# Optimization experiments

Hardware: AMD Instinct MI355X
Metric: run time of the kernel (lower is better)

## Reference

```python
import jax, jax.numpy as jnp
import numpy as np

EPS = 1e-6

def fexp(x, p):
    # signed power used in superquadric parametrization
    return jnp.sign(x) * (jnp.abs(x) + EPS) ** p

def quat_to_rot(q):
    q = q / (jnp.linalg.norm(q, axis=-1, keepdims=True) + EPS)
    w, x, y, z = q[..., 0], q[..., 1], q[..., 2], q[..., 3]
    R = jnp.stack([
        jnp.stack([1 - 2 * (y * y + z * z), 2 * (x * y - w * z), 2 * (x * z + w * y)], -1),
        jnp.stack([2 * (x * y + w * z), 1 - 2 * (x * x + z * z), 2 * (y * z - w * x)], -1),
        jnp.stack([2 * (x * z - w * y), 2 * (y * z + w * x), 1 - 2 * (x * x + y * y)], -1),
    ], -2)
    return R  # (..., 3, 3)

def setup_inputs() -> dict:
    key = jax.random.key(0)
    ks = jax.random.split(key, 9)
    B, M, S, N = 8, 16, 100, 2048
    pcl = jax.random.normal(ks[0], (B, N, 3), jnp.float32)
    translations = 0.5 * jax.random.normal(ks[1], (B, M, 3), jnp.float32)
    rotations = jax.random.normal(ks[2], (B, M, 4), jnp.float32)
    size = 0.2 + 0.6 * jax.random.uniform(ks[3], (B, M, 3), jnp.float32)
    shape_eps = 0.4 + 1.2 * jax.random.uniform(ks[4], (B, M, 2), jnp.float32)
    deformations = 0.6 * jax.random.uniform(ks[5], (B, M, 2), jnp.float32) - 0.3
    probabilities = jax.random.uniform(ks[6], (B, M), jnp.float32, 0.05, 0.95)
    etas = jax.random.uniform(ks[7], (S,), jnp.float32, -np.pi / 2, np.pi / 2)
    omegas = jax.random.uniform(ks[8], (S,), jnp.float32, -np.pi, np.pi)
    return {"pcl": pcl, "translations": translations, "rotations": rotations,
            "size": size, "shape_eps": shape_eps, "deformations": deformations,
            "probabilities": probabilities, "etas": etas, "omegas": omegas}

def reference(pcl, translations, rotations, size, shape_eps, deformations, probabilities, etas, omegas):
    B, N, _ = pcl.shape
    M = translations.shape[1]
    # transform pcl into primitive-centric frames: (B,N,M,3)
    R = quat_to_rot(rotations)                                   # (B,M,3,3)
    d = pcl[:, :, None, :] - translations[:, None, :, :]         # (B,N,M,3)
    pcl_t = jnp.einsum('bmij,bnmj->bnmi', R, d)                  # (B,N,M,3)
    # sample superquadric surfaces: (B,M,S,3)
    e1 = shape_eps[..., 0:1]; e2 = shape_eps[..., 1:2]           # (B,M,1)
    a1 = size[..., 0:1]; a2 = size[..., 1:2]; a3 = size[..., 2:3]
    ce = fexp(jnp.cos(etas)[None, None, :], e1)
    se = fexp(jnp.sin(etas)[None, None, :], e1)
    cw = fexp(jnp.cos(omegas)[None, None, :], e2)
    sw = fexp(jnp.sin(omegas)[None, None, :], e2)
    x = a1 * ce * cw; y = a2 * ce * sw; z = a3 * se              # (B,M,S)
    # tapering deformation
    fx = deformations[..., 0:1] * z / a3 + 1.0
    fy = deformations[..., 1:2] * z / a3 + 1.0
    points = jnp.stack([fx * x, fy * y, z], -1)                  # (B,M,S,3)
    # pairwise squared distances: (B,M,S,N)
    diff = points[:, :, :, None, :] - jnp.transpose(pcl_t, (0, 2, 1, 3))[:, :, None, :, :]
    dist = jnp.sum(diff * diff, -1)
    # --- pcl_to_prim loss ---
    dmin = jnp.transpose(jnp.min(dist, axis=2), (0, 2, 1))       # (B,N,M)
    idx = jnp.argsort(dmin, axis=-1)
    distance = jnp.take_along_axis(dmin, idx, axis=-1)
    probs_g = jax.vmap(lambda p, i: p[i])(probabilities, idx)    # (B,N,M)
    neg_cp = jnp.cumprod(1.0 - probs_g, axis=-1)
    neg_cp = jnp.concatenate([jnp.ones_like(neg_cp[..., :1]), neg_cp[..., :-1]], -1)
    minprob = probs_g * neg_cp
    pcl_to_prim = jnp.sum(distance * minprob) / (B * N)
    # --- prim_to_pcl loss ---
    dminN = jnp.min(dist, axis=3)                                # (B,M,S)
    dminN = jnp.where(dminN >= 1e30, 0.0, dminN)
    s0, s1, s2 = size[..., 0], size[..., 1], size[..., 2]
    area = 4 * np.pi * ((s0 * s1) ** 1.6 / 3 + (s0 * s2) ** 1.6 / 3 + (s1 * s2) ** 1.6 / 3) ** 0.625
    area = M * area / jnp.sum(area, axis=-1, keepdims=True)
    prim_to_pcl = jnp.sum(jnp.mean(dminN, -1) * area) / (B * M)
    # regularizer weights are zero (regularizer_type=None path) -> regs = 0
    return pcl_to_prim + prim_to_pcl
```

## Files before the change

### kernel.cpp

```cpp
#include <hip/hip_runtime.h>
#include <math.h>

#define EPSF 1e-6f

constexpr int B = 8, N = 2048, M = 16, S = 100;
constexpr int MAIN_BLOCKS = B * (N / 64);
constexpr int PRIM_BLOCKS = B * M * 2;
constexpr int TOTAL_BLOCKS = MAIN_BLOCKS + PRIM_BLOCKS;
constexpr int NPART = MAIN_BLOCKS * 4 + PRIM_BLOCKS;

typedef float v2f __attribute__((ext_vector_type(2)));

__device__ __forceinline__ float hw_exp2(float x) { return __builtin_amdgcn_exp2f(x); }
__device__ __forceinline__ float hw_log2(float x) { return __builtin_amdgcn_logf(x); }

__device__ __forceinline__ float fexp_d(float x, float p) {
    float sg = (x > 0.f) ? 1.f : ((x < 0.f) ? -1.f : 0.f);
    return sg * __powf(fabsf(x) + EPSF, p);
}

__device__ __forceinline__ float sgn_d(float x) {
    return (x > 0.f) ? 1.f : ((x < 0.f) ? -1.f : 0.f);
}

__device__ __forceinline__ void quat_R(const float* __restrict__ rot, int bm, float R[9]) {
    float w = rot[bm * 4 + 0], x = rot[bm * 4 + 1], y = rot[bm * 4 + 2], z = rot[bm * 4 + 3];
    float inv = 1.0f / (sqrtf(w * w + x * x + y * y + z * z) + EPSF);
    w *= inv; x *= inv; y *= inv; z *= inv;
    R[0] = 1.f - 2.f * (y * y + z * z); R[1] = 2.f * (x * y - w * z); R[2] = 2.f * (x * z + w * y);
    R[3] = 2.f * (x * y + w * z); R[4] = 1.f - 2.f * (x * x + z * z); R[5] = 2.f * (y * z - w * x);
    R[6] = 2.f * (x * z - w * y); R[7] = 2.f * (y * z + w * x); R[8] = 1.f - 2.f * (x * x + y * y);
}

__device__ __forceinline__ float4 surf_point(
    const float* __restrict__ sizep, const float* __restrict__ seps,
    const float* __restrict__ deform, const float* __restrict__ etas,
    const float* __restrict__ omegas, int bm, int s)
{
    float e1 = seps[bm * 2 + 0], e2 = seps[bm * 2 + 1];
    float a1 = sizep[bm * 3 + 0], a2 = sizep[bm * 3 + 1], a3 = sizep[bm * 3 + 2];
    float d0 = deform[bm * 2 + 0], d1 = deform[bm * 2 + 1];
    float se_, ce_, sw_, cw_;
    __sincosf(etas[s], &se_, &ce_);
    __sincosf(omegas[s], &sw_, &cw_);
    float ce = fexp_d(ce_, e1);
    float se = fexp_d(se_, e1);
    float cw = fexp_d(cw_, e2);
    float sw = fexp_d(sw_, e2);
    float x = a1 * ce * cw;
    float y = a2 * ce * sw;
    float z = a3 * se;
    float fx = d0 * (z / a3) + 1.0f;
    float fy = d1 * (z / a3) + 1.0f;
    float4 P;
    P.x = fx * x; P.y = fy * y; P.z = z;
    P.w = P.x * P.x + P.y * P.y + P.z * P.z;
    return P;
}

__global__ __launch_bounds__(256) void k_all(
    const float* __restrict__ pcl, const float* __restrict__ trans,
    const float* __restrict__ rot, const float* __restrict__ sizep,
    const float* __restrict__ seps, const float* __restrict__ deform,
    const float* __restrict__ probs,
    const float* __restrict__ etas, const float* __restrict__ omegas,
    float* __restrict__ part, unsigned int* __restrict__ flags,
    float* __restrict__ out)
{
    __shared__ float4 pts[S * M];
    __shared__ float trig[S * 8];
    __shared__ float sbuf[20];

    int t = threadIdx.x;

    if (blockIdx.x < MAIN_BLOCKS) {
        int b  = blockIdx.x >> 5;
        int n0 = (blockIdx.x & 31) * 64;

        if (t < S) {
            float se_, ce_, sw_, cw_;
            __sincosf(etas[t], &se_, &ce_);
            __sincosf(omegas[t], &sw_, &cw_);
            trig[t * 8 + 0] = hw_log2(fabsf(ce_) + EPSF);
            trig[t * 8 + 1] = sgn_d(ce_);
            trig[t * 8 + 2] = hw_log2(fabsf(se_) + EPSF);
            trig[t * 8 + 3] = sgn_d(se_);
            trig[t * 8 + 4] = hw_log2(fabsf(cw_) + EPSF);
            trig[t * 8 + 5] = sgn_d(cw_);
            trig[t * 8 + 6] = hw_log2(fabsf(sw_) + EPSF);
            trig[t * 8 + 7] = sgn_d(sw_);
        }
        __syncthreads();

        for (int i = t; i < S * M; i += 256) {
            int s = i >> 4, mm = i & 15;
            int bmi = b * M + mm;
            float e1 = seps[bmi * 2 + 0], e2 = seps[bmi * 2 + 1];
            float a1 = sizep[bmi * 3 + 0], a2 = sizep[bmi * 3 + 1], a3 = sizep[bmi * 3 + 2];
            float d0 = deform[bmi * 2 + 0], d1 = deform[bmi * 2 + 1];
            float ce = trig[s * 8 + 1] * hw_exp2(e1 * trig[s * 8 + 0]);
            float se = trig[s * 8 + 3] * hw_exp2(e1 * trig[s * 8 + 2]);
            float cw = trig[s * 8 + 5] * hw_exp2(e2 * trig[s * 8 + 4]);
            float sw = trig[s * 8 + 7] * hw_exp2(e2 * trig[s * 8 + 6]);
            float x = a1 * ce * cw;
            float y = a2 * ce * sw;
            float z = a3 * se;
            float fx = fmaf(d0, se, 1.0f);
            float fy = fmaf(d1, se, 1.0f);
            float4 P;
            P.x = fx * x; P.y = fy * y; P.z = z;
            P.w = P.x * P.x + P.y * P.y + P.z * P.z;
            pts[i] = P;
        }
        __syncthreads();

        int m  = t & 15;
        int nl = t >> 4;
        int bm = b * M + m;
        float R[9];
        quat_R(rot, bm, R);
        float tx = trans[bm * 3 + 0], ty = trans[bm * 3 + 1], tz = trans[bm * 3 + 2];

        v2f mx2[2], my2[2], mz2[2], dmin2[2];
        float psq[4];
#pragma unroll
        for (int j = 0; j < 4; j++) {
            int n = n0 + nl + 16 * j;
            float px = pcl[(b * N + n) * 3 + 0];
            float py = pcl[(b * N + n) * 3 + 1];
            float pz = pcl[(b * N + n) * 3 + 2];
            float dx = px - tx, dy = py - ty, dz = pz - tz;
            float X = R[0] * dx + R[1] * dy + R[2] * dz;
            float Y = R[3] * dx + R[4] * dy + R[5] * dz;
            float Z = R[6] * dx + R[7] * dy + R[8] * dz;
            mx2[j >> 1][j & 1] = -2.f * X;
            my2[j >> 1][j & 1] = -2.f * Y;
            mz2[j >> 1][j & 1] = -2.f * Z;
            psq[j] = X * X + Y * Y + Z * Z;
            dmin2[j >> 1][j & 1] = 3.4e38f;
        }

        auto compute4 = [&](const float4* P4) {
#pragma unroll
            for (int u = 0; u < 4; u++) {
                float4 P = P4[u];
                v2f vx = {P.x, P.x}, vy = {P.y, P.y}, vz = {P.z, P.z}, vw = {P.w, P.w};
#pragma unroll
                for (int p = 0; p < 2; p++) {
                    v2f d = __builtin_elementwise_fma(vx, mx2[p], vw);
                    d = __builtin_elementwise_fma(vy, my2[p], d);
                    d = __builtin_elementwise_fma(vz, mz2[p], d);
                    dmin2[p] = __builtin_elementwise_min(dmin2[p], d);
                }
            }
        };

        float4 Pa[4], Pb[4];
#pragma unroll
        for (int u = 0; u < 4; u++) Pa[u] = pts[u * M + m];
        for (int g = 0; g < 24; g += 2) {
#pragma unroll
            for (int u = 0; u < 4; u++) Pb[u] = pts[(4 * (g + 1) + u) * M + m];
            compute4(Pa);
#pragma unroll
            for (int u = 0; u < 4; u++) Pa[u] = pts[(4 * (g + 2) + u) * M + m];
            compute4(Pb);
        }
        compute4(Pa);

        float ompr[16];
#pragma unroll
        for (int k = 0; k < 16; k++) ompr[k] = 1.f - probs[b * M + k];
        float pv  = probs[bm];
        float acc = 0.f;
#pragma unroll
        for (int j = 0; j < 4; j++) {
            float key = dmin2[j >> 1][j & 1] + psq[j];
            float prod = 1.f;
#pragma unroll
            for (int k = 0; k < 16; k++) {
                float bk = __shfl(key, k, 16);
                bool before = (bk < key) || (bk == key && k < m);
                prod *= before ? ompr[k] : 1.f;
            }
            acc += key * pv * prod;
        }
        for (int off = 32; off >= 1; off >>= 1) acc += __shfl_down(acc, off);
        if ((t & 63) == 0)
            __hip_atomic_store(&part[blockIdx.x * 4 + (t >> 6)],
                               acc * (1.0f / (B * N)),
                               __ATOMIC_RELAXED, __HIP_MEMORY_SCOPE_AGENT);
        __syncthreads();
        if (t == 0)
            __hip_atomic_store(&flags[blockIdx.x], 1u,
                               __ATOMIC_RELEASE, __HIP_MEMORY_SCOPE_AGENT);
    } else if (blockIdx.x < TOTAL_BLOCKS) {
        int pb = blockIdx.x - MAIN_BLOCKS;
        int bm = pb >> 1, q = pb & 1;
        int b = bm >> 4, m = bm & 15;
        int s0 = q * 50;

        float4* spts = pts;
        float* sarea = sbuf;
        float* wsum  = sbuf + 16;

        if (t < 50) spts[t] = surf_point(sizep, seps, deform, etas, omegas, bm, s0 + t);
        if (t >= 64 && t < 64 + M) {
            int mm = t - 64;
            float s0s = sizep[(b * M + mm) * 3 + 0];
            float s1s = sizep[(b * M + mm) * 3 + 1];
            float s2s = sizep[(b * M + mm) * 3 + 2];
            float tt = __powf(s0s * s1s, 1.6f) / 3.f + __powf(s0s * s2s, 1.6f) / 3.f
                     + __powf(s1s * s2s, 1.6f) / 3.f;
            sarea[mm] = 4.0f * 3.14159265358979323846f * __powf(tt, 0.625f);
        }
        __syncthreads();

        float R[9];
        quat_R(rot, bm, R);
        float tx = trans[bm * 3 + 0], ty = trans[bm * 3 + 1], tz = trans[bm * 3 + 2];

        int w = t >> 6, lane = t & 63;
        int cnt = (w < 2) ? 13 : 12;
        int off = (w < 2) ? w * 13 : 26 + (w - 2) * 12;

        v2f px2[7], py2[7], pz2[7], mins2[7];
#pragma unroll
        for (int k = 0; k < 14; k++) {
            int sl = (k < cnt) ? (off + k) : off;
            float4 P = spts[sl];
            px2[k >> 1][k & 1] = P.x;
            py2[k >> 1][k & 1] = P.y;
            pz2[k >> 1][k & 1] = P.z;
            mins2[k >> 1][k & 1] = 3.4e38f;
        }

        const float* pcb = pcl + b * N * 3 + lane * 3;

#define LOADG(x0,y0,z0,x1,y1,z1,x2,y2,z2,x3,y3,z3, g)            \
        { const float* p_ = pcb + (g) * 768;                     \
          x0 = p_[0];   y0 = p_[1];   z0 = p_[2];                \
          x1 = p_[192]; y1 = p_[193]; z1 = p_[194];              \
          x2 = p_[384]; y2 = p_[385]; z2 = p_[386];              \
          x3 = p_[576]; y3 = p_[577]; z3 = p_[578]; }

#define COMP1(cx,cy,cz)                                          \
        { float dx = (cx) - tx, dy = (cy) - ty, dz = (cz) - tz;  \
          float X = R[0] * dx + R[1] * dy + R[2] * dz;           \
          float Y = R[3] * dx + R[4] * dy + R[5] * dz;           \
          float Z = R[6] * dx + R[7] * dy + R[8] * dz;           \
          float Xsq = X * X + Y * Y + Z * Z;                     \
          v2f vmX = {-2.f * X, -2.f * X}, vmY = {-2.f * Y, -2.f * Y}; \
          v2f vmZ = {-2.f * Z, -2.f * Z}, vXq = {Xsq, Xsq};      \
          _Pragma("unroll")                                      \
          for (int k = 0; k < 7; k++) {                          \
              v2f d = __builtin_elementwise_fma(px2[k], vmX, vXq); \
              d = __builtin_elementwise_fma(py2[k], vmY, d);     \
              d = __builtin_elementwise_fma(pz2[k], vmZ, d);     \
              mins2[k] = __builtin_elementwise_min(mins2[k], d); \
          } }

#define COMPG(x0,y0,z0,x1,y1,z1,x2,y2,z2,x3,y3,z3)               \
        COMP1(x0,y0,z0) COMP1(x1,y1,z1) COMP1(x2,y2,z2) COMP1(x3,y3,z3)

        float a0x,a0y,a0z,a1x,a1y,a1z,a2x,a2y,a2z,a3x,a3y,a3z;
        float b0x,b0y,b0z,b1x,b1y,b1z,b2x,b2y,b2z,b3x,b3y,b3z;

        LOADG(a0x,a0y,a0z,a1x,a1y,a1z,a2x,a2y,a2z,a3x,a3y,a3z, 0)
        LOADG(b0x,b0y,b0z,b1x,b1y,b1z,b2x,b2y,b2z,b3x,b3y,b3z, 1)
        COMPG(a0x,a0y,a0z,a1x,a1y,a1z,a2x,a2y,a2z,a3x,a3y,a3z)
        LOADG(a0x,a0y,a0z,a1x,a1y,a1z,a2x,a2y,a2z,a3x,a3y,a3z, 2)
        COMPG(b0x,b0y,b0z,b1x,b1y,b1z,b2x,b2y,b2z,b3x,b3y,b3z)
        LOADG(b0x,b0y,b0z,b1x,b1y,b1z,b2x,b2y,b2z,b3x,b3y,b3z, 3)
        COMPG(a0x,a0y,a0z,a1x,a1y,a1z,a2x,a2y,a2z,a3x,a3y,a3z)
        LOADG(a0x,a0y,a0z,a1x,a1y,a1z,a2x,a2y,a2z,a3x,a3y,a3z, 4)
        COMPG(b0x,b0y,b0z,b1x,b1y,b1z,b2x,b2y,b2z,b3x,b3y,b3z)
        LOADG(b0x,b0y,b0z,b1x,b1y,b1z,b2x,b2y,b2z,b3x,b3y,b3z, 5)
        COMPG(a0x,a0y,a0z,a1x,a1y,a1z,a2x,a2y,a2z,a3x,a3y,a3z)
        LOADG(a0x,a0y,a0z,a1x,a1y,a1z,a2x,a2y,a2z,a3x,a3y,a3z, 6)
        COMPG(b0x,b0y,b0z,b1x,b1y,b1z,b2x,b2y,b2z,b3x,b3y,b3z)
        LOADG(b0x,b0y,b0z,b1x,b1y,b1z,b2x,b2y,b2z,b3x,b3y,b3z, 7)
        COMPG(a0x,a0y,a0z,a1x,a1y,a1z,a2x,a2y,a2z,a3x,a3y,a3z)
        COMPG(b0x,b0y,b0z,b1x,b1y,b1z,b2x,b2y,b2z,b3x,b3y,b3z)

#undef LOADG
#undef COMP1
#undef COMPG

        float sum = 0.f;
#pragma unroll
        for (int k = 0; k < 14; k++) {
            float v = mins2[k >> 1][k & 1];
            for (int o = 32; o >= 1; o >>= 1) v = fminf(v, __shfl_down(v, o));
            int sl = (k < cnt) ? (off + k) : off;
            v += spts[sl].w;
            sum += (k < cnt) ? v : 0.f;
        }

        if (lane == 0) wsum[w] = sum;
        __syncthreads();
        if (t == 0) {
            float total = wsum[0] + wsum[1] + wsum[2] + wsum[3];
            float asum = 0.f;
            for (int mm = 0; mm < M; mm++) asum += sarea[mm];
            float area = (float)M * sarea[m] / asum;
            __hip_atomic_store(&part[MAIN_BLOCKS * 4 + pb],
                               total * area * (1.0f / (S * B * M)),
                               __ATOMIC_RELAXED, __HIP_MEMORY_SCOPE_AGENT);
            __hip_atomic_store(&flags[blockIdx.x], 1u,
                               __ATOMIC_RELEASE, __HIP_MEMORY_SCOPE_AGENT);
        }
    } else {
        if (t >= 64) return;
        for (int i = t; i < TOTAL_BLOCKS; i += 64) {
            while (__hip_atomic_load(&flags[i], __ATOMIC_ACQUIRE,
                                     __HIP_MEMORY_SCOPE_AGENT) != 1u)
                __builtin_amdgcn_s_sleep(2);
        }
        __threadfence();
        float ssum = 0.f;
        for (int i = t; i < NPART; i += 64)
            ssum += __hip_atomic_load(&part[i], __ATOMIC_RELAXED,
                                      __HIP_MEMORY_SCOPE_AGENT);
        for (int off = 32; off >= 1; off >>= 1) ssum += __shfl_down(ssum, off);
        if (t == 0) out[0] = ssum;
        for (int i = t; i < TOTAL_BLOCKS; i += 64)
            __hip_atomic_store(&flags[i], 0u, __ATOMIC_RELAXED,
                               __HIP_MEMORY_SCOPE_AGENT);
    }
}

extern "C" void kernel_launch(void* const* d_in, const int* in_sizes, int n_in,
                              void* d_out, int out_size, void* d_ws, size_t ws_size,
                              hipStream_t stream)
{
    const float* pcl    = (const float*)d_in[0];
    const float* trans  = (const float*)d_in[1];
    const float* rot    = (const float*)d_in[2];
    const float* sizep  = (const float*)d_in[3];
    const float* seps   = (const float*)d_in[4];
    const float* deform = (const float*)d_in[5];
    const float* probs  = (const float*)d_in[6];
    const float* etas   = (const float*)d_in[7];
    const float* omegas = (const float*)d_in[8];
    float* out = (float*)d_out;
    float* partials = (float*)d_ws;
    unsigned int* flags = (unsigned int*)((char*)d_ws + 8192);

    k_all<<<TOTAL_BLOCKS + 1, 256, 0, stream>>>(pcl, trans, rot, sizep, seps,
                                                deform, probs, etas, omegas,
                                                partials, flags, out);
}
```

Before: 89.19 us.

## Hoist global loads, per-thread primitive params, deeper LDS prefetch, merge final reducer

```diff
diff --git a/kernel.cpp b/kernel.cpp
--- a/kernel.cpp
+++ b/kernel.cpp
@@ -23,13 +23,16 @@
     return (x > 0.f) ? 1.f : ((x < 0.f) ? -1.f : 0.f);
 }
 
-__device__ __forceinline__ void quat_R(const float* __restrict__ rot, int bm, float R[9]) {
-    float w = rot[bm * 4 + 0], x = rot[bm * 4 + 1], y = rot[bm * 4 + 2], z = rot[bm * 4 + 3];
+__device__ __forceinline__ void quat_Rv(float w, float x, float y, float z, float R[9]) {
     float inv = 1.0f / (sqrtf(w * w + x * x + y * y + z * z) + EPSF);
     w *= inv; x *= inv; y *= inv; z *= inv;
     R[0] = 1.f - 2.f * (y * y + z * z); R[1] = 2.f * (x * y - w * z); R[2] = 2.f * (x * z + w * y);
     R[3] = 2.f * (x * y + w * z); R[4] = 1.f - 2.f * (x * x + z * z); R[5] = 2.f * (y * z - w * x);
     R[6] = 2.f * (x * z - w * y); R[7] = 2.f * (y * z + w * x); R[8] = 1.f - 2.f * (x * x + y * y);
+}
+
+__device__ __forceinline__ void quat_R(const float* __restrict__ rot, int bm, float R[9]) {
+    quat_Rv(rot[bm * 4 + 0], rot[bm * 4 + 1], rot[bm * 4 + 2], rot[bm * 4 + 3], R);
 }
 
 __device__ __forceinline__ float4 surf_point(
@@ -68,7 +71,7 @@
     float* __restrict__ out)
 {
     __shared__ float4 pts[S * M];
-    __shared__ float trig[S * 8];
+    __shared__ __align__(16) float trig[S * 8];
     __shared__ float sbuf[20];
 
     int t = threadIdx.x;
@@ -76,60 +79,70 @@
     if (blockIdx.x < MAIN_BLOCKS) {
         int b  = blockIdx.x >> 5;
         int n0 = (blockIdx.x & 31) * 64;
-
+        int m  = t & 15;
+        int nl = t >> 4;
+        int bm = b * M + m;
+
+        float qw = rot[bm * 4 + 0], qx = rot[bm * 4 + 1];
+        float qy = rot[bm * 4 + 2], qz = rot[bm * 4 + 3];
+        float tx = trans[bm * 3 + 0], ty = trans[bm * 3 + 1], tz = trans[bm * 3 + 2];
+        float plx[4], ply[4], plz[4];
+#pragma unroll
+        for (int j = 0; j < 4; j++) {
+            int n = n0 + nl + 16 * j;
+            plx[j] = pcl[(b * N + n) * 3 + 0];
+            ply[j] = pcl[(b * N + n) * 3 + 1];
+            plz[j] = pcl[(b * N + n) * 3 + 2];
+        }
+        float pv = probs[bm];
+
+        float4* trig4 = (float4*)trig;
         if (t < S) {
             float se_, ce_, sw_, cw_;
             __sincosf(etas[t], &se_, &ce_);
             __sincosf(omegas[t], &sw_, &cw_);
-            trig[t * 8 + 0] = hw_log2(fabsf(ce_) + EPSF);
-            trig[t * 8 + 1] = sgn_d(ce_);
-            trig[t * 8 + 2] = hw_log2(fabsf(se_) + EPSF);
-            trig[t * 8 + 3] = sgn_d(se_);
-            trig[t * 8 + 4] = hw_log2(fabsf(cw_) + EPSF);
-            trig[t * 8 + 5] = sgn_d(cw_);
-            trig[t * 8 + 6] = hw_log2(fabsf(sw_) + EPSF);
-            trig[t * 8 + 7] = sgn_d(sw_);
-        }
-        __syncthreads();
-
-        for (int i = t; i < S * M; i += 256) {
-            int s = i >> 4, mm = i & 15;
-            int bmi = b * M + mm;
-            float e1 = seps[bmi * 2 + 0], e2 = seps[bmi * 2 + 1];
-            float a1 = sizep[bmi * 3 + 0], a2 = sizep[bmi * 3 + 1], a3 = sizep[bmi * 3 + 2];
-            float d0 = deform[bmi * 2 + 0], d1 = deform[bmi * 2 + 1];
-            float ce = trig[s * 8 + 1] * hw_exp2(e1 * trig[s * 8 + 0]);
-            float se = trig[s * 8 + 3] * hw_exp2(e1 * trig[s * 8 + 2]);
-            float cw = trig[s * 8 + 5] * hw_exp2(e2 * trig[s * 8 + 4]);
-            float sw = trig[s * 8 + 7] * hw_exp2(e2 * trig[s * 8 + 6]);
-            float x = a1 * ce * cw;
-            float y = a2 * ce * sw;
-            float z = a3 * se;
-            float fx = fmaf(d0, se, 1.0f);
-            float fy = fmaf(d1, se, 1.0f);
-            float4 P;
-            P.x = fx * x; P.y = fy * y; P.z = z;
-            P.w = P.x * P.x + P.y * P.y + P.z * P.z;
-            pts[i] = P;
-        }
-        __syncthreads();
-
-        int m  = t & 15;
-        int nl = t >> 4;
-        int bm = b * M + m;
+            float4 tA, tB;
+            tA.x = hw_log2(fabsf(ce_) + EPSF); tA.y = sgn_d(ce_);
+            tA.z = hw_log2(fabsf(se_) + EPSF); tA.w = sgn_d(se_);
+            tB.x = hw_log2(fabsf(cw_) + EPSF); tB.y = sgn_d(cw_);
+            tB.z = hw_log2(fabsf(sw_) + EPSF); tB.w = sgn_d(sw_);
+            trig4[t * 2 + 0] = tA;
+            trig4[t * 2 + 1] = tB;
+        }
+        __syncthreads();
+
+        {
+            float e1 = seps[bm * 2 + 0], e2 = seps[bm * 2 + 1];
+            float a1 = sizep[bm * 3 + 0], a2 = sizep[bm * 3 + 1], a3 = sizep[bm * 3 + 2];
+            float d0 = deform[bm * 2 + 0], d1 = deform[bm * 2 + 1];
+            for (int s = nl; s < S; s += 16) {
+                float4 tA = trig4[s * 2 + 0];
+                float4 tB = trig4[s * 2 + 1];
+                float ce = tA.y * hw_exp2(e1 * tA.x);
+                float se = tA.w * hw_exp2(e1 * tA.z);
+                float cw = tB.y * hw_exp2(e2 * tB.x);
+                float sw = tB.w * hw_exp2(e2 * tB.z);
+                float x = a1 * ce * cw;
+                float y = a2 * ce * sw;
+                float z = a3 * se;
+                float fx = fmaf(d0, se, 1.0f);
+                float fy = fmaf(d1, se, 1.0f);
+                float4 P;
+                P.x = fx * x; P.y = fy * y; P.z = z;
+                P.w = P.x * P.x + P.y * P.y + P.z * P.z;
+                pts[s * M + m] = P;
+            }
+        }
+        __syncthreads();
+
         float R[9];
-        quat_R(rot, bm, R);
-        float tx = trans[bm * 3 + 0], ty = trans[bm * 3 + 1], tz = trans[bm * 3 + 2];
+        quat_Rv(qw, qx, qy, qz, R);
 
         v2f mx2[2], my2[2], mz2[2], dmin2[2];
         float psq[4];
 #pragma unroll
         for (int j = 0; j < 4; j++) {
-            int n = n0 + nl + 16 * j;
-            float px = pcl[(b * N + n) * 3 + 0];
-            float py = pcl[(b * N + n) * 3 + 1];
-            float pz = pcl[(b * N + n) * 3 + 2];
-            float dx = px - tx, dy = py - ty, dz = pz - tz;
+            float dx = plx[j] - tx, dy = ply[j] - ty, dz = plz[j] - tz;
             float X = R[0] * dx + R[1] * dy + R[2] * dz;
             float Y = R[3] * dx + R[4] * dy + R[5] * dz;
             float Z = R[6] * dx + R[7] * dy + R[8] * dz;
@@ -154,24 +167,28 @@
                 }
             }
         };
-
-        float4 Pa[4], Pb[4];
-#pragma unroll
-        for (int u = 0; u < 4; u++) Pa[u] = pts[u * M + m];
-        for (int g = 0; g < 24; g += 2) {
-#pragma unroll
-            for (int u = 0; u < 4; u++) Pb[u] = pts[(4 * (g + 1) + u) * M + m];
-            compute4(Pa);
-#pragma unroll
-            for (int u = 0; u < 4; u++) Pa[u] = pts[(4 * (g + 2) + u) * M + m];
-            compute4(Pb);
-        }
-        compute4(Pa);
+        auto load8 = [&](float4* dst, int sbase) {
+#pragma unroll
+            for (int u = 0; u < 8; u++) dst[u] = pts[(sbase + u) * M + m];
+        };
+
+        float4 Abank[8], Bbank[8];
+        load8(Abank, 0);
+        for (int gp = 0; gp < 6; gp++) {
+            load8(Bbank, (2 * gp + 1) * 8);
+            compute4(Abank); compute4(Abank + 4);
+            if (gp < 5) load8(Abank, (2 * gp + 2) * 8);
+            else {
+#pragma unroll
+                for (int u = 0; u < 4; u++) Abank[u] = pts[(96 + u) * M + m];
+            }
+            compute4(Bbank); compute4(Bbank + 4);
+        }
+        compute4(Abank);
 
         float ompr[16];
 #pragma unroll
         for (int k = 0; k < 16; k++) ompr[k] = 1.f - probs[b * M + k];
-        float pv  = probs[bm];
         float acc = 0.f;
 #pragma unroll
         for (int j = 0; j < 4; j++) {
@@ -194,7 +211,7 @@
         if (t == 0)
             __hip_atomic_store(&flags[blockIdx.x], 1u,
                                __ATOMIC_RELEASE, __HIP_MEMORY_SCOPE_AGENT);
-    } else if (blockIdx.x < TOTAL_BLOCKS) {
+    } else {
         int pb = blockIdx.x - MAIN_BLOCKS;
         int bm = pb >> 1, q = pb & 1;
         int b = bm >> 4, m = bm & 15;
@@ -310,23 +327,24 @@
             __hip_atomic_store(&flags[blockIdx.x], 1u,
                                __ATOMIC_RELEASE, __HIP_MEMORY_SCOPE_AGENT);
         }
-    } else {
-        if (t >= 64) return;
-        for (int i = t; i < TOTAL_BLOCKS; i += 64) {
-            while (__hip_atomic_load(&flags[i], __ATOMIC_ACQUIRE,
-                                     __HIP_MEMORY_SCOPE_AGENT) != 1u)
-                __builtin_amdgcn_s_sleep(2);
-        }
-        __threadfence();
-        float ssum = 0.f;
-        for (int i = t; i < NPART; i += 64)
-            ssum += __hip_atomic_load(&part[i], __ATOMIC_RELAXED,
-                                      __HIP_MEMORY_SCOPE_AGENT);
-        for (int off = 32; off >= 1; off >>= 1) ssum += __shfl_down(ssum, off);
-        if (t == 0) out[0] = ssum;
-        for (int i = t; i < TOTAL_BLOCKS; i += 64)
-            __hip_atomic_store(&flags[i], 0u, __ATOMIC_RELAXED,
-                               __HIP_MEMORY_SCOPE_AGENT);
+
+        if (blockIdx.x == TOTAL_BLOCKS - 1 && t < 64) {
+            for (int i = t; i < TOTAL_BLOCKS; i += 64) {
+                while (__hip_atomic_load(&flags[i], __ATOMIC_ACQUIRE,
+                                         __HIP_MEMORY_SCOPE_AGENT) != 1u)
+                    __builtin_amdgcn_s_sleep(2);
+            }
+            __threadfence();
+            float ssum = 0.f;
+            for (int i = t; i < NPART; i += 64)
+                ssum += __hip_atomic_load(&part[i], __ATOMIC_RELAXED,
+                                          __HIP_MEMORY_SCOPE_AGENT);
+            for (int off = 32; off >= 1; off >>= 1) ssum += __shfl_down(ssum, off);
+            if (t == 0) out[0] = ssum;
+            for (int i = t; i < TOTAL_BLOCKS; i += 64)
+                __hip_atomic_store(&flags[i], 0u, __ATOMIC_RELAXED,
+                                   __HIP_MEMORY_SCOPE_AGENT);
+        }
     }
 }
 
@@ -347,7 +365,7 @@
     float* partials = (float*)d_ws;
     unsigned int* flags = (unsigned int*)((char*)d_ws + 8192);
 
-    k_all<<<TOTAL_BLOCKS + 1, 256, 0, stream>>>(pcl, trans, rot, sizep, seps,
-                                                deform, probs, etas, omegas,
-                                                partials, flags, out);
-}
+    k_all<<<TOTAL_BLOCKS, 256, 0, stream>>>(pcl, trans, rot, sizep, seps,
+                                            deform, probs, etas, omegas,
+                                            partials, flags, out);
+}
```

Result: no change. 88.25 us, median of 2 (-1.1%).
